# Kernel optimization log

Measured on AMD Instinct MI355X. Metric: run time of the kernel, lower is better.

## Reference

```python
import jax, jax.numpy as jnp
import numpy as np

N_OBS = 6000
N_X = 6000
D_FEAT = 16
N_DOM = 3


def _block_ranges(n, d):
    b = np.linspace(0, n, d + 1).astype(np.int32)
    return jnp.asarray(np.stack([b[:-1], b[1:]], axis=1))  # [d,2] (start,end)


def setup_inputs() -> dict:
    key = jax.random.key(0)
    ks = jax.random.split(key, 6)
    xobs = jax.random.normal(ks[0], (N_OBS, D_FEAT), jnp.float32)
    x = jax.random.normal(ks[1], (N_X, D_FEAT), jnp.float32)
    w = jnp.round(jax.random.uniform(ks[2], (N_X, 1), jnp.float32))  # binary treatment
    alpha0 = jax.random.uniform(ks[3], (N_OBS, 1), jnp.float32)
    alpha1 = jax.random.uniform(ks[4], (N_OBS, 1), jnp.float32)
    n_pairs = N_DOM * (N_DOM - 1) // 2
    transfer_factor_logit = 0.1 * jax.random.normal(ks[5], (n_pairs,), jnp.float32)
    raw_lengthscale = jnp.zeros((), jnp.float32)  # gpytorch raw param; softplus(0)~0.693
    return {
        "xobs": xobs, "x": x, "w": w,
        "alpha0": alpha0, "alpha1": alpha1,
        "transfer_factor_logit": transfer_factor_logit,
        "raw_lengthscale": raw_lengthscale,
        "domain_ranges_obs": _block_ranges(N_OBS, N_DOM),
        "domain_ranges_x": _block_ranges(N_X, N_DOM),
    }


def _matern52(x1, x2, lengthscale):
    # gpytorch MaternKernel(nu=5/2): k(d)=(1+sqrt5*d+5/3*d^2)exp(-sqrt5*d), d=||x1-x2||/ls
    x1 = x1 / lengthscale
    x2 = x2 / lengthscale
    sq = (jnp.sum(x1 * x1, 1)[:, None] + jnp.sum(x2 * x2, 1)[None, :]
          - 2.0 * (x1 @ x2.T))
    d = jnp.sqrt(jnp.maximum(sq, 1e-12))
    s5d = jnp.sqrt(jnp.asarray(5.0, d.dtype)) * d
    return (1.0 + s5d + (5.0 / 3.0) * d * d) * jnp.exp(-s5d)


def _domain_ids(n, ranges):
    # contiguous sorted partition: id = #starts <= idx  - 1
    idx = jnp.arange(n)
    return jnp.sum(idx[:, None] >= ranges[None, :, 0], axis=1) - 1


def reference(xobs, x, w, alpha0, alpha1, transfer_factor_logit,
              raw_lengthscale, domain_ranges_obs, domain_ranges_x):
    ls = jax.nn.softplus(raw_lengthscale)
    M = _matern52(xobs, x, ls)                       # [N_obs, N_x]
    # pairwise transfer factor matrix F[di,dj]: 1 on diagonal, sigmoid(logit_n)
    # for pair n enumerated as (i<j) row-major, matching the original loop order
    tf = jax.nn.sigmoid(transfer_factor_logit)
    iu, ju = np.triu_indices(N_DOM, 1)
    F = jnp.ones((N_DOM, N_DOM), M.dtype).at[iu, ju].set(tf).at[ju, iu].set(tf)
    dom_o = _domain_ids(xobs.shape[0], domain_ranges_obs)   # [N_obs]
    dom_x = _domain_ids(x.shape[0], domain_ranges_x)        # [N_x]
    K = M * F[dom_o[:, None], dom_x[None, :]]               # fused transfer blend
    f0 = alpha0[:, 0] @ K                                   # [N_x]
    f1 = alpha1[:, 0] @ K
    wv = w.reshape(-1)
    return wv * f0 + (1.0 - wv) * f1
```

## Files before the change

kernel.cpp:

```cpp
#include <hip/hip_runtime.h>
#include <math.h>

typedef _Float16 f16x8 __attribute__((ext_vector_type(8)));
typedef float    f32x4 __attribute__((ext_vector_type(4)));

__global__ __launch_bounds__(256) void prep_split(
    const float* __restrict__ xobs, const float* __restrict__ x,
    const float* __restrict__ alpha0, const float* __restrict__ alpha1,
    const float* __restrict__ tfl, const float* __restrict__ rawls,
    const int* __restrict__ rngo,
    _Float16* __restrict__ ap,
    _Float16* __restrict__ bh,
    _Float16* __restrict__ bl,
    float* __restrict__ no5, float* __restrict__ nx5,
    float* __restrict__ a0f, float* __restrict__ a1f,
    int n_obs, int n_x)
{
    const int i = blockIdx.x * 256 + threadIdx.x;
    const float r  = rawls[0];
    const float ls = fmaxf(r, 0.f) + log1pf(__expf(-fabsf(r)));
    const float s5_ls2 = 5.f / (ls * ls);

    if (i < n_obs) {
        float s = 0.f;
        #pragma unroll
        for (int k = 0; k < 16; ++k) {
            const float v = xobs[(size_t)i * 16 + k];
            s = fmaf(v, v, s);
            const _Float16 h = (_Float16)v;
            ap[(size_t)i * 32 + k]      = h;
            ap[(size_t)i * 32 + 16 + k] = (_Float16)(v - (float)h);
        }
        no5[i] = s * s5_ls2;

        const float t0 = 1.f / (1.f + __expf(-tfl[0]));
        const float t1 = 1.f / (1.f + __expf(-tfl[1]));
        const float t2 = 1.f / (1.f + __expf(-tfl[2]));
        const int dom = (i >= rngo[2] ? 1 : 0) + (i >= rngo[4] ? 1 : 0);
        const float F0 = (dom == 0) ? 1.f : ((dom == 1) ? t0 : t1);
        const float F1 = (dom == 0) ? t0  : ((dom == 1) ? 1.f : t2);
        const float F2 = (dom == 0) ? t1  : ((dom == 1) ? t2  : 1.f);
        const float av0 = alpha0[i], av1 = alpha1[i];
        a0f[i]              = av0 * F0;
        a0f[n_obs + i]      = av0 * F1;
        a0f[2 * n_obs + i]  = av0 * F2;
        a1f[i]              = av1 * F0;
        a1f[n_obs + i]      = av1 * F1;
        a1f[2 * n_obs + i]  = av1 * F2;
    }
    if (i < n_x) {
        float s = 0.f;
        #pragma unroll
        for (int k = 0; k < 16; ++k) {
            const float v = x[(size_t)i * 16 + k];
            s = fmaf(v, v, s);
            const _Float16 h = (_Float16)v;
            bh[(size_t)i * 16 + k] = h;
            bl[(size_t)i * 16 + k] = (_Float16)(v - (float)h);
        }
        nx5[i] = s * s5_ls2;
    }
}

__global__ __launch_bounds__(256, 4) void matern_mfma(
    const _Float16* __restrict__ ap, const _Float16* __restrict__ bh,
    const _Float16* __restrict__ bl,
    const float* __restrict__ no5, const float* __restrict__ nx5,
    const float* __restrict__ a0f, const float* __restrict__ a1f,
    const float* __restrict__ rawls, const int* __restrict__ rngx,
    float* __restrict__ f01, int n_obs, int n_x, int ntiles_i, int tiles_per_chunk)
{
    const int wave = threadIdx.x >> 6;
    const int lane = threadIdx.x & 63;
    const int njt  = n_x >> 4;
    const int jt   = blockIdx.x * 4 + wave;
    if (jt >= njt) return;
    const int g16 = lane >> 4;
    const int l16 = lane & 15;
    const int j   = jt * 16 + l16;

    const f16x8 B1 = *(const f16x8*)(bh + (size_t)j * 16 + (g16 & 1) * 8);
    f16x8 B2 = f16x8{0, 0, 0, 0, 0, 0, 0, 0};
    if (g16 < 2) B2 = *(const f16x8*)(bl + (size_t)j * 16 + g16 * 8);

    const float r  = rawls[0];
    const float ls = fmaxf(r, 0.f) + log1pf(__expf(-fabsf(r)));
    const float c2_5 = -10.f / (ls * ls);
    const float nx5j = nx5[j];

    const int dxj = (j >= rngx[2] ? 1 : 0) + (j >= rngx[4] ? 1 : 0);
    const float* __restrict__ a0p = a0f + (size_t)dxj * n_obs;
    const float* __restrict__ a1p = a1f + (size_t)dxj * n_obs;

    const float C13  = 1.f / 3.f;
    const float NL2E = -1.4426950408889634f;

    float s0 = 0.f, s1 = 0.f;
    const int it0 = blockIdx.y * tiles_per_chunk;
    const int it1 = min(it0 + tiles_per_chunk, ntiles_i);

    #define TAIL4(ACC, NOV, A0V, A1V)                                        \
        _Pragma("unroll")                                                    \
        for (int rr = 0; rr < 4; ++rr) {                                     \
            float u = fmaf(c2_5, (ACC)[rr], (NOV)[rr] + nx5j);               \
            u = fmaxf(u, 1e-11f);                                            \
            const float rs   = __frsqrt_rn(u);                               \
            const float s5d  = u * rs;                          \
            const float poly = fmaf(C13, u, 1.f + s5d);                      \
            const float e    = __builtin_amdgcn_exp2f(NL2E * s5d);           \
            const float m    = poly * e;                                     \
            s0 = fmaf((A0V)[rr], m, s0);                                     \
            s1 = fmaf((A1V)[rr], m, s1);                                     \
        }

    int it = it0;
    for (; it + 1 < it1; it += 2) {
        const int ia = it * 16, ib = ia + 16;
        const f16x8 Aa = *(const f16x8*)(ap + (size_t)(ia + l16) * 32 + g16 * 8);
        const f16x8 Ab = *(const f16x8*)(ap + (size_t)(ib + l16) * 32 + g16 * 8);
        const int ra = ia + g16 * 4, rb = ib + g16 * 4;
        const f32x4 nova = *(const f32x4*)(no5 + ra);
        const f32x4 novb = *(const f32x4*)(no5 + rb);
        const f32x4 a0a  = *(const f32x4*)(a0p + ra);
        const f32x4 a0b  = *(const f32x4*)(a0p + rb);
        const f32x4 a1a  = *(const f32x4*)(a1p + ra);
        const f32x4 a1b  = *(const f32x4*)(a1p + rb);

        f32x4 acca = {0.f, 0.f, 0.f, 0.f};
        acca = __builtin_amdgcn_mfma_f32_16x16x32_f16(Aa, B1, acca, 0, 0, 0);
        acca = __builtin_amdgcn_mfma_f32_16x16x32_f16(Aa, B2, acca, 0, 0, 0);
        f32x4 accb = {0.f, 0.f, 0.f, 0.f};
        accb = __builtin_amdgcn_mfma_f32_16x16x32_f16(Ab, B1, accb, 0, 0, 0);
        accb = __builtin_amdgcn_mfma_f32_16x16x32_f16(Ab, B2, accb, 0, 0, 0);

        TAIL4(acca, nova, a0a, a1a)
        TAIL4(accb, novb, a0b, a1b)
    }
    if (it < it1) {
        const int ia = it * 16;
        const f16x8 Aa = *(const f16x8*)(ap + (size_t)(ia + l16) * 32 + g16 * 8);
        const int ra = ia + g16 * 4;
        const f32x4 nova = *(const f32x4*)(no5 + ra);
        const f32x4 a0a  = *(const f32x4*)(a0p + ra);
        const f32x4 a1a  = *(const f32x4*)(a1p + ra);
        f32x4 acca = {0.f, 0.f, 0.f, 0.f};
        acca = __builtin_amdgcn_mfma_f32_16x16x32_f16(Aa, B1, acca, 0, 0, 0);
        acca = __builtin_amdgcn_mfma_f32_16x16x32_f16(Aa, B2, acca, 0, 0, 0);
        TAIL4(acca, nova, a0a, a1a)
    }
    #undef TAIL4

    s0 += __shfl_xor(s0, 16, 64);
    s0 += __shfl_xor(s0, 32, 64);
    s1 += __shfl_xor(s1, 16, 64);
    s1 += __shfl_xor(s1, 32, 64);
    if (g16 == 0) {
        atomicAdd(&f01[j], s0);
        atomicAdd(&f01[n_x + j], s1);
    }
}

__global__ void combine_out(const float* __restrict__ w,
                            const float* __restrict__ f01,
                            float* __restrict__ out, int n_x)
{
    const int j = blockIdx.x * 256 + threadIdx.x;
    if (j < n_x) {
        const float wv = w[j];
        out[j] = wv * f01[j] + (1.f - wv) * f01[n_x + j];
    }
}

extern "C" void kernel_launch(void* const* d_in, const int* in_sizes, int n_in,
                              void* d_out, int out_size, void* d_ws, size_t ws_size,
                              hipStream_t stream)
{
    const float* xobs = (const float*)d_in[0];
    const float* x    = (const float*)d_in[1];
    const float* w    = (const float*)d_in[2];
    const float* a0   = (const float*)d_in[3];
    const float* a1   = (const float*)d_in[4];
    const float* tfl  = (const float*)d_in[5];
    const float* rls  = (const float*)d_in[6];
    const int*   rngo = (const int*)d_in[7];
    const int*   rngx = (const int*)d_in[8];

    const int n_obs = in_sizes[0] / 16;
    const int n_x   = in_sizes[1] / 16;

    char* p = (char*)d_ws;
    auto take = [&](size_t bytes) { char* q = p; p += (bytes + 255) & ~(size_t)255; return q; };
    float*     f01 = (float*)    take(sizeof(float) * 2 * (size_t)n_x);
    _Float16*  ap  = (_Float16*) take(sizeof(_Float16) * 32 * (size_t)n_obs);
    _Float16*  bh  = (_Float16*) take(sizeof(_Float16) * 16 * (size_t)n_x);
    _Float16*  bl  = (_Float16*) take(sizeof(_Float16) * 16 * (size_t)n_x);
    float*     no5 = (float*)    take(sizeof(float) * (size_t)n_obs);
    float*     nx5 = (float*)    take(sizeof(float) * (size_t)n_x);
    float*     a0f = (float*)    take(sizeof(float) * 3 * (size_t)n_obs);
    float*     a1f = (float*)    take(sizeof(float) * 3 * (size_t)n_obs);

    (void)hipMemsetAsync(f01, 0, sizeof(float) * 2 * (size_t)n_x, stream);

    const int nmax = (n_obs > n_x) ? n_obs : n_x;
    prep_split<<<(nmax + 255) / 256, 256, 0, stream>>>(
        xobs, x, a0, a1, tfl, rls, rngo, ap, bh, bl, no5, nx5, a0f, a1f, n_obs, n_x);

    const int njt = n_x / 16;
    const int ntiles_i = n_obs / 16;
    const int tiles_per_chunk = 15;
    const int gy = (ntiles_i + tiles_per_chunk - 1) / tiles_per_chunk;
    dim3 grid((njt + 3) / 4, gy);
    matern_mfma<<<grid, 256, 0, stream>>>(ap, bh, bl, no5, nx5, a0f, a1f, rls,
                                          rngx, f01, n_obs, n_x,
                                          ntiles_i, tiles_per_chunk);

    combine_out<<<(n_x + 255) / 256, 256, 0, stream>>>(w, f01, (float*)d_out, n_x);
}
```

Before: 101.6 us.

## Parallelize prep over feature lanes, drop tile unroll, raise matern occupancy

The prep kernel now gives each feature element its own thread (16 threads per row) and reduces the squared norm with wave shuffles, so global loads and stores are coalesced instead of strided per-row loops. The main kernel's two-tile manual unroll is removed in favour of a simple loop, and launch bounds now request 8 waves per SIMD instead of 4. This trades instruction-level parallelism for occupancy and lower register pressure, and adds a larger prep grid.

Result: no change. 99.93 us (-1.6%).

```diff
diff --git a/kernel.cpp b/kernel.cpp
--- a/kernel.cpp
+++ b/kernel.cpp
@@ -4,65 +4,68 @@
 typedef _Float16 f16x8 __attribute__((ext_vector_type(8)));
 typedef float    f32x4 __attribute__((ext_vector_type(4)));
 
-__global__ __launch_bounds__(256) void prep_split(
+__global__ __launch_bounds__(256) void prep_all(
     const float* __restrict__ xobs, const float* __restrict__ x,
     const float* __restrict__ alpha0, const float* __restrict__ alpha1,
     const float* __restrict__ tfl, const float* __restrict__ rawls,
     const int* __restrict__ rngo,
-    _Float16* __restrict__ ap,
-    _Float16* __restrict__ bh,
-    _Float16* __restrict__ bl,
+    _Float16* __restrict__ ap, _Float16* __restrict__ bh, _Float16* __restrict__ bl,
     float* __restrict__ no5, float* __restrict__ nx5,
     float* __restrict__ a0f, float* __restrict__ a1f,
     int n_obs, int n_x)
 {
-    const int i = blockIdx.x * 256 + threadIdx.x;
-    const float r  = rawls[0];
-    const float ls = fmaxf(r, 0.f) + log1pf(__expf(-fabsf(r)));
+    const int t   = threadIdx.x;
+    const int r   = t >> 4;
+    const int k   = t & 15;
+    const int row = blockIdx.x * 16 + r;
+
+    const float rv = rawls[0];
+    const float ls = fmaxf(rv, 0.f) + log1pf(__expf(-fabsf(rv)));
     const float s5_ls2 = 5.f / (ls * ls);
 
-    if (i < n_obs) {
-        float s = 0.f;
-        #pragma unroll
-        for (int k = 0; k < 16; ++k) {
-            const float v = xobs[(size_t)i * 16 + k];
-            s = fmaf(v, v, s);
-            const _Float16 h = (_Float16)v;
-            ap[(size_t)i * 32 + k]      = h;
-            ap[(size_t)i * 32 + 16 + k] = (_Float16)(v - (float)h);
+    if (row < n_obs) {
+        const float v = xobs[(size_t)row * 16 + k];
+        float nv = v * v;
+        nv += __shfl_xor(nv, 1, 64);
+        nv += __shfl_xor(nv, 2, 64);
+        nv += __shfl_xor(nv, 4, 64);
+        nv += __shfl_xor(nv, 8, 64);
+        const _Float16 h = (_Float16)v;
+        ap[(size_t)row * 32 + k]      = h;
+        ap[(size_t)row * 32 + 16 + k] = (_Float16)(v - (float)h);
+        if (k == 0) no5[row] = nv * s5_ls2;
+        if (k == 1) {
+            const float t0 = 1.f / (1.f + __expf(-tfl[0]));
+            const float t1 = 1.f / (1.f + __expf(-tfl[1]));
+            const float t2 = 1.f / (1.f + __expf(-tfl[2]));
+            const int dom = (row >= rngo[2] ? 1 : 0) + (row >= rngo[4] ? 1 : 0);
+            const float F0 = (dom == 0) ? 1.f : ((dom == 1) ? t0 : t1);
+            const float F1 = (dom == 0) ? t0  : ((dom == 1) ? 1.f : t2);
+            const float F2 = (dom == 0) ? t1  : ((dom == 1) ? t2  : 1.f);
+            const float av0 = alpha0[row], av1 = alpha1[row];
+            a0f[row]             = av0 * F0;
+            a0f[n_obs + row]     = av0 * F1;
+            a0f[2 * n_obs + row] = av0 * F2;
+            a1f[row]             = av1 * F0;
+            a1f[n_obs + row]     = av1 * F1;
+            a1f[2 * n_obs + row] = av1 * F2;
         }
-        no5[i] = s * s5_ls2;
-
-        const float t0 = 1.f / (1.f + __expf(-tfl[0]));
-        const float t1 = 1.f / (1.f + __expf(-tfl[1]));
-        const float t2 = 1.f / (1.f + __expf(-tfl[2]));
-        const int dom = (i >= rngo[2] ? 1 : 0) + (i >= rngo[4] ? 1 : 0);
-        const float F0 = (dom == 0) ? 1.f : ((dom == 1) ? t0 : t1);
-        const float F1 = (dom == 0) ? t0  : ((dom == 1) ? 1.f : t2);
-        const float F2 = (dom == 0) ? t1  : ((dom == 1) ? t2  : 1.f);
-        const float av0 = alpha0[i], av1 = alpha1[i];
-        a0f[i]              = av0 * F0;
-        a0f[n_obs + i]      = av0 * F1;
-        a0f[2 * n_obs + i]  = av0 * F2;
-        a1f[i]              = av1 * F0;
-        a1f[n_obs + i]      = av1 * F1;
-        a1f[2 * n_obs + i]  = av1 * F2;
     }
-    if (i < n_x) {
-        float s = 0.f;
-        #pragma unroll
-        for (int k = 0; k < 16; ++k) {
-            const float v = x[(size_t)i * 16 + k];
-            s = fmaf(v, v, s);
-            const _Float16 h = (_Float16)v;
-            bh[(size_t)i * 16 + k] = h;
-            bl[(size_t)i * 16 + k] = (_Float16)(v - (float)h);
-        }
-        nx5[i] = s * s5_ls2;
+    if (row < n_x) {
+        const float v = x[(size_t)row * 16 + k];
+        float nv = v * v;
+        nv += __shfl_xor(nv, 1, 64);
+        nv += __shfl_xor(nv, 2, 64);
+        nv += __shfl_xor(nv, 4, 64);
+        nv += __shfl_xor(nv, 8, 64);
+        const _Float16 h = (_Float16)v;
+        bh[(size_t)row * 16 + k] = h;
+        bl[(size_t)row * 16 + k] = (_Float16)(v - (float)h);
+        if (k == 0) nx5[row] = nv * s5_ls2;
     }
 }
 
-__global__ __launch_bounds__(256, 4) void matern_mfma(
+__global__ __launch_bounds__(256, 8) void matern_mfma(
     const _Float16* __restrict__ ap, const _Float16* __restrict__ bh,
     const _Float16* __restrict__ bl,
     const float* __restrict__ no5, const float* __restrict__ nx5,
@@ -83,8 +86,8 @@
     f16x8 B2 = f16x8{0, 0, 0, 0, 0, 0, 0, 0};
     if (g16 < 2) B2 = *(const f16x8*)(bl + (size_t)j * 16 + g16 * 8);
 
-    const float r  = rawls[0];
-    const float ls = fmaxf(r, 0.f) + log1pf(__expf(-fabsf(r)));
+    const float rv = rawls[0];
+    const float ls = fmaxf(rv, 0.f) + log1pf(__expf(-fabsf(rv)));
     const float c2_5 = -10.f / (ls * ls);
     const float nx5j = nx5[j];
 
@@ -99,56 +102,31 @@
     const int it0 = blockIdx.y * tiles_per_chunk;
     const int it1 = min(it0 + tiles_per_chunk, ntiles_i);
 
-    #define TAIL4(ACC, NOV, A0V, A1V)                                        \
-        _Pragma("unroll")                                                    \
-        for (int rr = 0; rr < 4; ++rr) {                                     \
-            float u = fmaf(c2_5, (ACC)[rr], (NOV)[rr] + nx5j);               \
-            u = fmaxf(u, 1e-11f);                                            \
-            const float rs   = __frsqrt_rn(u);                               \
-            const float s5d  = u * rs;                          \
-            const float poly = fmaf(C13, u, 1.f + s5d);                      \
-            const float e    = __builtin_amdgcn_exp2f(NL2E * s5d);           \
-            const float m    = poly * e;                                     \
-            s0 = fmaf((A0V)[rr], m, s0);                                     \
-            s1 = fmaf((A1V)[rr], m, s1);                                     \
-        }
-
-    int it = it0;
-    for (; it + 1 < it1; it += 2) {
-        const int ia = it * 16, ib = ia + 16;
-        const f16x8 Aa = *(const f16x8*)(ap + (size_t)(ia + l16) * 32 + g16 * 8);
-        const f16x8 Ab = *(const f16x8*)(ap + (size_t)(ib + l16) * 32 + g16 * 8);
-        const int ra = ia + g16 * 4, rb = ib + g16 * 4;
-        const f32x4 nova = *(const f32x4*)(no5 + ra);
-        const f32x4 novb = *(const f32x4*)(no5 + rb);
-        const f32x4 a0a  = *(const f32x4*)(a0p + ra);
-        const f32x4 a0b  = *(const f32x4*)(a0p + rb);
-        const f32x4 a1a  = *(const f32x4*)(a1p + ra);
-        const f32x4 a1b  = *(const f32x4*)(a1p + rb);
-
-        f32x4 acca = {0.f, 0.f, 0.f, 0.f};
-        acca = __builtin_amdgcn_mfma_f32_16x16x32_f16(Aa, B1, acca, 0, 0, 0);
-        acca = __builtin_amdgcn_mfma_f32_16x16x32_f16(Aa, B2, acca, 0, 0, 0);
-        f32x4 accb = {0.f, 0.f, 0.f, 0.f};
-        accb = __builtin_amdgcn_mfma_f32_16x16x32_f16(Ab, B1, accb, 0, 0, 0);
-        accb = __builtin_amdgcn_mfma_f32_16x16x32_f16(Ab, B2, accb, 0, 0, 0);
-
-        TAIL4(acca, nova, a0a, a1a)
-        TAIL4(accb, novb, a0b, a1b)
-    }
-    if (it < it1) {
+    for (int it = it0; it < it1; ++it) {
         const int ia = it * 16;
         const f16x8 Aa = *(const f16x8*)(ap + (size_t)(ia + l16) * 32 + g16 * 8);
         const int ra = ia + g16 * 4;
-        const f32x4 nova = *(const f32x4*)(no5 + ra);
-        const f32x4 a0a  = *(const f32x4*)(a0p + ra);
-        const f32x4 a1a  = *(const f32x4*)(a1p + ra);
-        f32x4 acca = {0.f, 0.f, 0.f, 0.f};
-        acca = __builtin_amdgcn_mfma_f32_16x16x32_f16(Aa, B1, acca, 0, 0, 0);
-        acca = __builtin_amdgcn_mfma_f32_16x16x32_f16(Aa, B2, acca, 0, 0, 0);
-        TAIL4(acca, nova, a0a, a1a)
+        const f32x4 nov = *(const f32x4*)(no5 + ra);
+        const f32x4 a0v = *(const f32x4*)(a0p + ra);
+        const f32x4 a1v = *(const f32x4*)(a1p + ra);
+
+        f32x4 acc = {0.f, 0.f, 0.f, 0.f};
+        acc = __builtin_amdgcn_mfma_f32_16x16x32_f16(Aa, B1, acc, 0, 0, 0);
+        acc = __builtin_amdgcn_mfma_f32_16x16x32_f16(Aa, B2, acc, 0, 0, 0);
+
+        #pragma unroll
+        for (int rr = 0; rr < 4; ++rr) {
+            float u = fmaf(c2_5, acc[rr], nov[rr] + nx5j);
+            u = fmaxf(u, 1e-11f);
+            const float rs   = __frsqrt_rn(u);
+            const float s5d  = u * rs;
+            const float poly = fmaf(C13, u, 1.f + s5d);
+            const float e    = __builtin_amdgcn_exp2f(NL2E * s5d);
+            const float m    = poly * e;
+            s0 = fmaf(a0v[rr], m, s0);
+            s1 = fmaf(a1v[rr], m, s1);
+        }
     }
-    #undef TAIL4
 
     s0 += __shfl_xor(s0, 16, 64);
     s0 += __shfl_xor(s0, 32, 64);
@@ -202,7 +180,7 @@
     (void)hipMemsetAsync(f01, 0, sizeof(float) * 2 * (size_t)n_x, stream);
 
     const int nmax = (n_obs > n_x) ? n_obs : n_x;
-    prep_split<<<(nmax + 255) / 256, 256, 0, stream>>>(
+    prep_all<<<(nmax + 15) / 16, 256, 0, stream>>>(
         xobs, x, a0, a1, tfl, rls, rngo, ap, bh, bl, no5, nx5, a0f, a1f, n_obs, n_x);
 
     const int njt = n_x / 16;
```
